# Kernel optimization log

Measured on AMD Instinct MI355X. Metric: run time of the kernel, lower is better.

Reference implementation:

```python
import jax, jax.numpy as jnp
import numpy as np

N_NODES = 20000
N_EDGES = 320000
F_IN = 512
HID = 64
N_GRAPHS = 64
N_CLASSES = 5
SLOPE = 0.2      # PyG GATConv default negative_slope
EPS_BN = 1e-5


def setup_inputs() -> dict:
    key = jax.random.key(0)
    k = jax.random.split(key, 16)
    s = 0.05
    rn = lambda kk, sh: jax.random.normal(kk, sh, jnp.float32) * s
    return {
        "x": jax.random.normal(k[0], (N_NODES, F_IN), jnp.float32),
        "edge_index": jax.random.randint(k[1], (2, N_EDGES), 0, N_NODES, jnp.int32),
        "batch": jnp.sort(jax.random.randint(k[2], (N_NODES,), 0, N_GRAPHS, jnp.int32)),
        "W1": rn(k[3], (F_IN, 4 * HID)),
        "a1_src": rn(k[4], (4, HID)), "a1_dst": rn(k[5], (4, HID)),
        "b1": jnp.zeros((4 * HID,), jnp.float32),
        "bn1_gamma": jnp.ones((4 * HID,), jnp.float32), "bn1_beta": jnp.zeros((4 * HID,), jnp.float32),
        "bn1_mean": jnp.zeros((4 * HID,), jnp.float32), "bn1_var": jnp.ones((4 * HID,), jnp.float32),
        "W2": rn(k[6], (4 * HID, 4 * HID)),
        "a2_src": rn(k[7], (4, HID)), "a2_dst": rn(k[8], (4, HID)),
        "b2": jnp.zeros((4 * HID,), jnp.float32),
        "bn2_gamma": jnp.ones((4 * HID,), jnp.float32), "bn2_beta": jnp.zeros((4 * HID,), jnp.float32),
        "bn2_mean": jnp.zeros((4 * HID,), jnp.float32), "bn2_var": jnp.ones((4 * HID,), jnp.float32),
        "W3": rn(k[9], (4 * HID, HID)),
        "a3_src": rn(k[10], (1, HID)), "a3_dst": rn(k[11], (1, HID)),
        "b3": jnp.zeros((HID,), jnp.float32),
        "lin1_w": rn(k[12], (HID, HID // 2)), "lin1_b": jnp.zeros((HID // 2,), jnp.float32),
        "lin2_w": rn(k[13], (HID // 2, N_CLASSES)), "lin2_b": jnp.zeros((N_CLASSES,), jnp.float32),
    }


def _gat(x, src, dst, W, a_s, a_d, b, heads, concat):
    """PyG-style GATConv (eval mode, self-loops already in src/dst)."""
    n = x.shape[0]
    h = (x @ W).reshape(n, heads, -1)                         # [N,H,C]
    al_s = (h * a_s).sum(-1)                                  # [N,H]
    al_d = (h * a_d).sum(-1)                                  # [N,H]
    e = jax.nn.leaky_relu(al_s[src] + al_d[dst], SLOPE)       # [E,H]
    m = jax.lax.stop_gradient(jax.ops.segment_max(e, dst, num_segments=n))
    ee = jnp.exp(e - m[dst])
    denom = jax.ops.segment_sum(ee, dst, num_segments=n)      # [N,H]
    alpha = ee / (denom[dst] + 1e-16)                         # segment softmax over dst
    out = jax.ops.segment_sum(h[src] * alpha[:, :, None], dst, num_segments=n)  # [N,H,C]
    out = out.reshape(n, -1) if concat else out.mean(axis=1)
    return out + b


def _bn(x, g, b, m, v):  # BatchNorm1d, eval mode
    return (x - m) * jax.lax.rsqrt(v + EPS_BN) * g + b


def reference(x, edge_index, batch, W1, a1_src, a1_dst, b1, bn1_gamma, bn1_beta, bn1_mean, bn1_var, W2, a2_src, a2_dst, b2, bn2_gamma, bn2_beta, bn2_mean, bn2_var, W3, a3_src, a3_dst, b3, lin1_w, lin1_b, lin2_w, lin2_b):
    n = x.shape[0]
    loops = jnp.arange(n, dtype=edge_index.dtype)             # GATConv add_self_loops=True
    src = jnp.concatenate([edge_index[0], loops])
    dst = jnp.concatenate([edge_index[1], loops])
    h = _gat(x, src, dst, W1, a1_src, a1_dst, b1, 4, True)
    h = jax.nn.relu(_bn(h, bn1_gamma, bn1_beta, bn1_mean, bn1_var))
    h = _gat(h, src, dst, W2, a2_src, a2_dst, b2, 4, True)
    h = jax.nn.relu(_bn(h, bn2_gamma, bn2_beta, bn2_mean, bn2_var))
    h = jax.nn.relu(_gat(h, src, dst, W3, a3_src, a3_dst, b3, 1, False))
    sums = jax.ops.segment_sum(h, batch, num_segments=N_GRAPHS)
    cnt = jax.ops.segment_sum(jnp.ones((n, 1), h.dtype), batch, num_segments=N_GRAPHS)
    g = sums / jnp.maximum(cnt, 1.0)                          # global_mean_pool
    g = jax.nn.relu(g @ lin1_w + lin1_b)
    return g @ lin2_w + lin2_b
```

## Files before the change

### kernel.cpp

```cpp
#include <hip/hip_runtime.h>

#define N_NODES 20000
#define N_EDGES 320000
#define E_TOT   340000
#define N_GRAPHS 64
#define N_CLASSES 5
#define SLOPE 0.2f
#define EPS_BN 1e-5f

#define CB 96
#define NCH 209

typedef _Float16 v8h __attribute__((ext_vector_type(8)));
typedef float v4f __attribute__((ext_vector_type(4)));
typedef _Float16 v4h __attribute__((ext_vector_type(4)));

#define SPQ (N_NODES * 512 / 4)
#define W1E (512 * 256)
#define W2E (256 * 256)
#define W3E (256 * 64)
#define ALZ (80000 * 4 + 20000 * 2)
#define PREP_IDS (SPQ + W1E + W2E + W3E + N_NODES + N_NODES + N_GRAPHS * 64 + ALZ)

#define RELBASE 384
#define CTRL_INTS (RELBASE + 3 * 256)

__global__ __launch_bounds__(256) void k_prep(const float* __restrict__ x,
                                              _Float16* __restrict__ xh,
                                              const float* __restrict__ W1, _Float16* __restrict__ bt1,
                                              const float* __restrict__ W2, _Float16* __restrict__ bt2,
                                              const float* __restrict__ W3, _Float16* __restrict__ bt3,
                                              const int* __restrict__ batch, int* __restrict__ gstart,
                                              int* __restrict__ cnt, float* __restrict__ sums,
                                              float* __restrict__ albase) {
    int id = blockIdx.x * 256 + threadIdx.x;
    if (id < SPQ) {
        const float4 v = *(const float4*)(x + (size_t)id * 4);
        v4h h;
        h.x = (_Float16)v.x; h.y = (_Float16)v.y; h.z = (_Float16)v.z; h.w = (_Float16)v.w;
        *(v4h*)(xh + (size_t)id * 4) = h;
        return;
    }
    id -= SPQ;
    if (id < W1E) {
        const int K = 512, N = 256;
        int n = id / K, k = id - n * K;
        bt1[id] = (_Float16)W1[(size_t)k * N + n];
        return;
    }
    id -= W1E;
    if (id < W2E) {
        const int K = 256, N = 256;
        int n = id / K, k = id - n * K;
        bt2[id] = (_Float16)W2[(size_t)k * N + n];
        return;
    }
    id -= W2E;
    if (id < W3E) {
        const int K = 256, N = 64;
        int n = id / K, k = id - n * K;
        bt3[id] = (_Float16)W3[(size_t)k * N + n];
        return;
    }
    id -= W3E;
    if (id < N_NODES) {
        int i = id;
        int b = batch[i];
        if (i == 0) {
            for (int g = 0; g <= b; ++g) gstart[g] = 0;
        } else {
            int p = batch[i - 1];
            for (int g = p + 1; g <= b; ++g) gstart[g] = i;
        }
        if (i == N_NODES - 1) {
            for (int g = b + 1; g <= N_GRAPHS; ++g) gstart[g] = N_NODES;
        }
        return;
    }
    id -= N_NODES;
    if (id < N_NODES) { cnt[id] = 0; return; }
    id -= N_NODES;
    if (id < N_GRAPHS * 64) { sums[id] = 0.f; return; }
    id -= N_GRAPHS * 64;
    if (id < ALZ) albase[id] = 0.f;
}

__device__ __forceinline__ void gsync96(int* ctrl, int k, int bid) {
    int* arr = ctrl + k * CB;
    int* rel = ctrl + RELBASE + k * 256;
    __syncthreads();
    if (threadIdx.x == 0) {
        __builtin_amdgcn_fence(__ATOMIC_RELEASE, "agent");
        __hip_atomic_store(&arr[bid], 1, __ATOMIC_RELAXED, __HIP_MEMORY_SCOPE_AGENT);
    }
    if (bid == 0) {
        if ((int)threadIdx.x < CB) {
            while (__hip_atomic_load(&arr[threadIdx.x], __ATOMIC_RELAXED, __HIP_MEMORY_SCOPE_AGENT) == 0)
                __builtin_amdgcn_s_sleep(8);
        }
        __syncthreads();
        if (threadIdx.x < 8) {
            __hip_atomic_store(&rel[threadIdx.x * 32], 1, __ATOMIC_RELAXED, __HIP_MEMORY_SCOPE_AGENT);
        }
        if (threadIdx.x == 0)
            __builtin_amdgcn_fence(__ATOMIC_ACQUIRE, "agent");
    } else if (threadIdx.x == 0) {
        int* myrel = &rel[(bid & 7) * 32];
        while (__hip_atomic_load(myrel, __ATOMIC_RELAXED, __HIP_MEMORY_SCOPE_AGENT) == 0)
            __builtin_amdgcn_s_sleep(8);
        __builtin_amdgcn_fence(__ATOMIC_ACQUIRE, "agent");
    }
    __syncthreads();
}

__device__ void csr_build(const int* __restrict__ ei, int* __restrict__ cnt,
                          int* __restrict__ wptr, int* __restrict__ indptr,
                          int* __restrict__ esrc, int* __restrict__ blocksum,
                          int* __restrict__ ctrl, int bid, int tid, int* ssc) {
    for (int e = bid * 256 + tid; e < E_TOT; e += CB * 256) {
        int d = (e < N_EDGES) ? ei[N_EDGES + e] : (e - N_EDGES);
        atomicAdd(&cnt[d], 1);
    }
    gsync96(ctrl, 0, bid);
    const int i = bid * NCH + tid;
    const int active = (tid < NCH && i < N_NODES);
    int ls = active ? cnt[i] : 0;
    ssc[tid] = ls;
    __syncthreads();
    for (int off = 1; off < 256; off <<= 1) {
        int v = (tid >= off) ? ssc[tid - off] : 0;
        __syncthreads();
        ssc[tid] += v;
        __syncthreads();
    }
    const int epre = ssc[tid] - ls;
    if (tid == 255) blocksum[bid] = ssc[255];
    gsync96(ctrl, 1, bid);
    int boff = 0;
    for (int j = 0; j < bid; ++j) boff += blocksum[j];
    if (active) {
        const int run = boff + epre;
        indptr[i] = run;
        wptr[i] = run;
    }
    if (bid == 0 && tid == 0) indptr[N_NODES] = E_TOT;
    gsync96(ctrl, 2, bid);
    for (int e = bid * 256 + tid; e < E_TOT; e += CB * 256) {
        int s, d;
        if (e < N_EDGES) { s = ei[e]; d = ei[N_EDGES + e]; }
        else             { s = d = e - N_EDGES; }
        int pos = atomicAdd(&wptr[d], 1);
        esrc[pos] = s;
    }
}

template <int TN, int KK>
__device__ void gemm_tile(const _Float16* __restrict__ A,
                          const _Float16* __restrict__ Bt,
                          _Float16* __restrict__ H,
                          const float* __restrict__ aw_s,
                          const float* __restrict__ aw_d,
                          float* __restrict__ als,
                          float* __restrict__ ald,
                          int HS, int N, int bx, int by, _Float16* lbh) {
    constexpr int NTB = 2 * TN;
    constexpr int NFRAG = 2 * NTB * 64;
    constexpr int NITER = NFRAG / 256;
    const int tid = threadIdx.x;
    const int wave = tid >> 6, lane = tid & 63;
    const int wr = wave >> 1, wc = wave & 1;
    const int q = lane >> 4, r = lane & 15;
    const int m0 = bx * 64 + wr * 32;
    const int n0 = by * (NTB * 16);
    size_t abase[2];
#pragma unroll
    for (int mi = 0; mi < 2; ++mi) {
        int ar = m0 + mi * 16 + r;
        if (ar >= N_NODES) ar = N_NODES - 1;
        abase[mi] = (size_t)ar * KK + q * 8;
    }
    size_t gaddr[NITER];
    int loff[NITER];
#pragma unroll
    for (int j = 0; j < NITER; ++j) {
        const int f = tid + j * 256;
        const int qq = f & 3;
        const int ss = (f >> 2) & 1;
        const int rr = (f >> 3) & 15;
        const int tt = f >> 7;
        gaddr[j] = (size_t)(n0 + tt * 16 + rr) * KK + ss * 32 + qq * 8;
        const int fi = (ss * NTB + tt) * 64 + qq * 16 + rr;
        loff[j] = fi * 8 + (fi >> 4) * 8;
    }
    v4f acc[2][TN];
#pragma unroll
    for (int mi = 0; mi < 2; ++mi)
#pragma unroll
        for (int t = 0; t < TN; ++t) acc[mi][t] = (v4f){0.f, 0.f, 0.f, 0.f};

    v8h ch[NITER];
#pragma unroll
    for (int j = 0; j < NITER; ++j) ch[j] = *(const v8h*)(Bt + gaddr[j]);

#pragma unroll
    for (int kc = 0; kc < KK; kc += 64) {
        __syncthreads();
#pragma unroll
        for (int j = 0; j < NITER; ++j) *(v8h*)&lbh[loff[j]] = ch[j];
        __syncthreads();
        if (kc + 64 < KK) {
#pragma unroll
            for (int j = 0; j < NITER; ++j) ch[j] = *(const v8h*)(Bt + gaddr[j] + kc + 64);
        }
#pragma unroll
        for (int ss = 0; ss < 2; ++ss) {
            v8h ah[2];
#pragma unroll
            for (int mi = 0; mi < 2; ++mi)
                ah[mi] = *(const v8h*)(A + abase[mi] + kc + ss * 32);
#pragma unroll
            for (int t = 0; t < TN; ++t) {
                const int fib = (ss * NTB + wc * TN + t) * 4 + q;
                const int off = (fib * 16 + r) * 8 + fib * 8;
                const v8h bh = *(const v8h*)&lbh[off];
#pragma unroll
                for (int mi = 0; mi < 2; ++mi)
                    acc[mi][t] = __builtin_amdgcn_mfma_f32_16x16x32_f16(ah[mi], bh, acc[mi][t], 0, 0, 0);
            }
        }
    }
#pragma unroll
    for (int mi = 0; mi < 2; ++mi)
#pragma unroll
        for (int t = 0; t < TN; ++t)
#pragma unroll
            for (int i = 0; i < 4; ++i) {
                const int row = m0 + mi * 16 + q * 4 + i;
                if (row < N_NODES) H[(size_t)row * N + n0 + (wc * TN + t) * 16 + r] = (_Float16)acc[mi][t][i];
            }
    const int colbase = n0 + wc * TN * 16;
    const int hd = colbase >> 6;
#pragma unroll
    for (int mi = 0; mi < 2; ++mi)
#pragma unroll
        for (int i = 0; i < 4; ++i) {
            float sp = 0.f, dp = 0.f;
#pragma unroll
            for (int t = 0; t < TN; ++t) {
                const int col = colbase + t * 16 + r;
                sp += acc[mi][t][i] * aw_s[col];
                dp += acc[mi][t][i] * aw_d[col];
            }
#pragma unroll
            for (int m = 1; m < 16; m <<= 1) {
                sp += __shfl_xor(sp, m, 64);
                dp += __shfl_xor(dp, m, 64);
            }
            const int row = m0 + mi * 16 + q * 4 + i;
            if (r == 0 && row < N_NODES) {
                atomicAdd(&als[row * HS + hd], sp);
                atomicAdd(&ald[row * HS + hd], dp);
            }
        }
}

__global__ __launch_bounds__(256) void k_p1(const int* __restrict__ ei,
                                            int* __restrict__ cnt, int* __restrict__ wptr,
                                            int* __restrict__ indptr, int* __restrict__ esrc,
                                            int* __restrict__ blocksum, int* __restrict__ ctrl,
                                            const _Float16* __restrict__ xh,
                                            const _Float16* __restrict__ bt1,
                                            _Float16* __restrict__ bufH,
                                            const float* __restrict__ a1s,
                                            const float* __restrict__ a1d,
                                            float* __restrict__ als1, float* __restrict__ ald1) {
    __shared__ __align__(16) char smraw[17472];
    const int bid = blockIdx.x;
    const int tid = threadIdx.x;
    if (bid < CB) {
        csr_build(ei, cnt, wptr, indptr, esrc, blocksum, ctrl, bid, tid, (int*)smraw);
    } else {
        const int t = bid - CB;
        if (t < 626) gemm_tile<4, 512>(xh, bt1, bufH, a1s, a1d, als1, ald1, 4, 256,
                                       t >> 1, t & 1, (_Float16*)smraw);
    }
}

template <int TN, int KK>
__global__ __launch_bounds__(256) void k_gemm(const _Float16* __restrict__ A,
                                              const _Float16* __restrict__ Bt,
                                              _Float16* __restrict__ H,
                                              const float* __restrict__ aw_s,
                                              const float* __restrict__ aw_d,
                                              float* __restrict__ als,
                                              float* __restrict__ ald,
                                              int HS, int N) {
    __shared__ __align__(16) char smraw[17472];
    gemm_tile<TN, KK>(A, Bt, H, aw_s, aw_d, als, ald, HS, N,
                      blockIdx.x, blockIdx.y, (_Float16*)smraw);
}

__global__ __launch_bounds__(256) void k_agg4(const _Float16* __restrict__ hin,
                                              const float* __restrict__ als,
                                              const float* __restrict__ ald,
                                              const int* __restrict__ indptr,
                                              const int* __restrict__ esrc,
                                              const float* __restrict__ bias,
                                              const float* __restrict__ gamma,
                                              const float* __restrict__ beta,
                                              const float* __restrict__ mean,
                                              const float* __restrict__ var,
                                              _Float16* __restrict__ pho) {
    __shared__ float lacc[2][64][4];
    __shared__ float lsm[2][64];
    const int pair = threadIdx.x >> 7;
    const int wv   = (threadIdx.x >> 6) & 1;
    const int lane = threadIdx.x & 63;
    const int n = blockIdx.x * 2 + pair;
    const int beg = indptr[n], end = indptr[n + 1];
    const int mid = beg + ((end - beg + 1) >> 1);
    const int e0 = wv ? mid : beg;
    const int e1 = wv ? end : mid;
    const int head = lane >> 4;
    const float aldn = ald[n * 4 + head];
    float4 acc = {0.f, 0.f, 0.f, 0.f};
    float sm = 0.f;
    const int c = lane * 4;
    int e = e0;
    for (; e + 3 < e1; e += 4) {
        const int s0 = esrc[e], s1 = esrc[e + 1], s2 = esrc[e + 2], s3 = esrc[e + 3];
        float v0 = als[s0 * 4 + head] + aldn;
        float v1 = als[s1 * 4 + head] + aldn;
        float v2 = als[s2 * 4 + head] + aldn;
        float v3 = als[s3 * 4 + head] + aldn;
        const v4h h0 = *(const v4h*)(hin + (size_t)s0 * 256 + c);
        const v4h h1 = *(const v4h*)(hin + (size_t)s1 * 256 + c);
        const v4h h2 = *(const v4h*)(hin + (size_t)s2 * 256 + c);
        const v4h h3 = *(const v4h*)(hin + (size_t)s3 * 256 + c);
        v0 = (v0 > 0.f) ? v0 : SLOPE * v0;
        v1 = (v1 > 0.f) ? v1 : SLOPE * v1;
        v2 = (v2 > 0.f) ? v2 : SLOPE * v2;
        v3 = (v3 > 0.f) ? v3 : SLOPE * v3;
        const float a0 = __expf(v0), a1 = __expf(v1), a2 = __expf(v2), a3 = __expf(v3);
        sm += (a0 + a1) + (a2 + a3);
        acc.x += a0 * (float)h0.x + a1 * (float)h1.x + a2 * (float)h2.x + a3 * (float)h3.x;
        acc.y += a0 * (float)h0.y + a1 * (float)h1.y + a2 * (float)h2.y + a3 * (float)h3.y;
        acc.z += a0 * (float)h0.z + a1 * (float)h1.z + a2 * (float)h2.z + a3 * (float)h3.z;
        acc.w += a0 * (float)h0.w + a1 * (float)h1.w + a2 * (float)h2.w + a3 * (float)h3.w;
    }
    for (; e < e1; ++e) {
        const int s0 = esrc[e];
        float v0 = als[s0 * 4 + head] + aldn;
        const v4h h0 = *(const v4h*)(hin + (size_t)s0 * 256 + c);
        v0 = (v0 > 0.f) ? v0 : SLOPE * v0;
        const float a0 = __expf(v0);
        sm += a0;
        acc.x += a0 * (float)h0.x; acc.y += a0 * (float)h0.y;
        acc.z += a0 * (float)h0.z; acc.w += a0 * (float)h0.w;
    }
    if (wv == 1) {
        lacc[pair][lane][0] = acc.x; lacc[pair][lane][1] = acc.y;
        lacc[pair][lane][2] = acc.z; lacc[pair][lane][3] = acc.w;
        lsm[pair][lane] = sm;
    }
    __syncthreads();
    if (wv == 0) {
        acc.x += lacc[pair][lane][0]; acc.y += lacc[pair][lane][1];
        acc.z += lacc[pair][lane][2]; acc.w += lacc[pair][lane][3];
        sm += lsm[pair][lane];
        const float invd = 1.f / (sm + 1e-16f);
        float y[4] = {acc.x * invd, acc.y * invd, acc.z * invd, acc.w * invd};
        v4h oh;
#pragma unroll
        for (int i = 0; i < 4; ++i) {
            float t = y[i] + bias[c + i];
            t = (t - mean[c + i]) * rsqrtf(var[c + i] + EPS_BN) * gamma[c + i] + beta[c + i];
            t = fmaxf(t, 0.f);
            oh[i] = (_Float16)t;
        }
        *(v4h*)(pho + (size_t)n * 256 + c) = oh;
    }
}

__global__ __launch_bounds__(256) void k_agg1(const _Float16* __restrict__ hin,
                                              const float* __restrict__ als,
                                              const float* __restrict__ ald,
                                              const int* __restrict__ indptr,
                                              const int* __restrict__ esrc,
                                              const float* __restrict__ bias,
                                              const int* __restrict__ batch,
                                              float* __restrict__ sums) {
    const int n = blockIdx.x * 4 + (threadIdx.x >> 6);
    const int lane = threadIdx.x & 63;
    const int beg = indptr[n], end = indptr[n + 1];
    const float aldn = ald[n];
    float acc = 0.f, sm = 0.f;
    int e = beg;
    for (; e + 3 < end; e += 4) {
        const int s0 = esrc[e], s1 = esrc[e + 1], s2 = esrc[e + 2], s3 = esrc[e + 3];
        float v0 = als[s0] + aldn;
        float v1 = als[s1] + aldn;
        float v2 = als[s2] + aldn;
        float v3 = als[s3] + aldn;
        const float h0 = (float)hin[(size_t)s0 * 64 + lane];
        const float h1 = (float)hin[(size_t)s1 * 64 + lane];
        const float h2 = (float)hin[(size_t)s2 * 64 + lane];
        const float h3 = (float)hin[(size_t)s3 * 64 + lane];
        v0 = (v0 > 0.f) ? v0 : SLOPE * v0;
        v1 = (v1 > 0.f) ? v1 : SLOPE * v1;
        v2 = (v2 > 0.f) ? v2 : SLOPE * v2;
        v3 = (v3 > 0.f) ? v3 : SLOPE * v3;
        const float a0 = __expf(v0), a1 = __expf(v1), a2 = __expf(v2), a3 = __expf(v3);
        sm += (a0 + a1) + (a2 + a3);
        acc += a0 * h0 + a1 * h1 + a2 * h2 + a3 * h3;
    }
    for (; e < end; ++e) {
        const int s0 = esrc[e];
        float v0 = als[s0] + aldn;
        const float h0 = (float)hin[(size_t)s0 * 64 + lane];
        v0 = (v0 > 0.f) ? v0 : SLOPE * v0;
        const float a0 = __expf(v0);
        sm += a0;
        acc += a0 * h0;
    }
    const float invd = 1.f / (sm + 1e-16f);
    const float val = fmaxf(acc * invd + bias[lane], 0.f);
    atomicAdd(&sums[batch[n] * 64 + lane], val);
}

__global__ void k_mlp(const float* __restrict__ sums, const int* __restrict__ gstart,
                      const float* __restrict__ w1, const float* __restrict__ b1,
                      const float* __restrict__ w2, const float* __restrict__ b2,
                      float* __restrict__ outp) {
    const int g = blockIdx.x;
    const int t = threadIdx.x;
    __shared__ float hid[32];
    const int cntn = gstart[g + 1] - gstart[g];
    const float inv = 1.f / (float)max(cntn, 1);
    float acc = b1[t];
    for (int c = 0; c < 64; ++c) acc += (sums[g * 64 + c] * inv) * w1[c * 32 + t];
    hid[t] = fmaxf(acc, 0.f);
    __syncthreads();
    if (t < N_CLASSES) {
        float o = b2[t];
        for (int k = 0; k < 32; ++k) o += hid[k] * w2[k * 5 + t];
        outp[g * 5 + t] = o;
    }
}

extern "C" void kernel_launch(void* const* d_in, const int* in_sizes, int n_in,
                              void* d_out, int out_size, void* d_ws, size_t ws_size,
                              hipStream_t stream) {
    const float* x        = (const float*)d_in[0];
    const int* edge_index = (const int*)d_in[1];
    const int* batch      = (const int*)d_in[2];
    const float* W1  = (const float*)d_in[3];
    const float* a1s = (const float*)d_in[4];
    const float* a1d = (const float*)d_in[5];
    const float* b1  = (const float*)d_in[6];
    const float* g1  = (const float*)d_in[7];
    const float* be1 = (const float*)d_in[8];
    const float* mu1 = (const float*)d_in[9];
    const float* va1 = (const float*)d_in[10];
    const float* W2  = (const float*)d_in[11];
    const float* a2s = (const float*)d_in[12];
    const float* a2d = (const float*)d_in[13];
    const float* b2  = (const float*)d_in[14];
    const float* g2  = (const float*)d_in[15];
    const float* be2 = (const float*)d_in[16];
    const float* mu2 = (const float*)d_in[17];
    const float* va2 = (const float*)d_in[18];
    const float* W3  = (const float*)d_in[19];
    const float* a3s = (const float*)d_in[20];
    const float* a3d = (const float*)d_in[21];
    const float* b3  = (const float*)d_in[22];
    const float* l1w = (const float*)d_in[23];
    const float* l1b = (const float*)d_in[24];
    const float* l2w = (const float*)d_in[25];
    const float* l2b = (const float*)d_in[26];
    float* out = (float*)d_out;

    char* w = (char*)d_ws;
    size_t off = 0;
    auto alloc = [&](size_t bytes) -> void* {
        void* p = w + off;
        off += (bytes + 255) & ~(size_t)255;
        return p;
    };
    _Float16* xh   = (_Float16*)alloc((size_t)N_NODES * 512 * 2);
    _Float16* phf  = xh;
    _Float16* bufH  = (_Float16*)alloc((size_t)N_NODES * 256 * 2);
    _Float16* bufH3 = (_Float16*)alloc((size_t)N_NODES * 64 * 2);
    _Float16* bt1 = (_Float16*)alloc((size_t)512 * 256 * 2);
    _Float16* bt2 = (_Float16*)alloc((size_t)256 * 256 * 2);
    _Float16* bt3 = (_Float16*)alloc((size_t)256 * 64 * 2);
    float* albase = (float*)alloc((size_t)ALZ * 4);
    float* als1 = albase;
    float* ald1 = albase + 80000;
    float* als2 = albase + 160000;
    float* ald2 = albase + 240000;
    float* als3 = albase + 320000;
    float* ald3 = albase + 340000;
    int* cnt      = (int*)alloc((size_t)N_NODES * 4);
    int* wptr     = (int*)alloc((size_t)N_NODES * 4);
    int* indptr   = (int*)alloc((size_t)(N_NODES + 1) * 4);
    int* esrc     = (int*)alloc((size_t)E_TOT * 4);
    int* gstart   = (int*)alloc((size_t)(N_GRAPHS + 1) * 4);
    float* sums   = (float*)alloc((size_t)N_GRAPHS * 64 * 4);
    int* blocksum = (int*)alloc((size_t)CB * 4);
    int* ctrl     = (int*)alloc((size_t)CTRL_INTS * 4);

    hipMemsetAsync(ctrl, 0, (size_t)CTRL_INTS * 4, stream);

    k_prep<<<(PREP_IDS + 255) / 256, 256, 0, stream>>>(x, xh, W1, bt1, W2, bt2, W3, bt3,
                                                       batch, gstart, cnt, sums, albase);
    k_p1<<<CB + 626, 256, 0, stream>>>(edge_index, cnt, wptr, indptr, esrc, blocksum, ctrl,
                                       xh, bt1, bufH, a1s, a1d, als1, ald1);
    k_agg4<<<N_NODES / 2, 256, 0, stream>>>(bufH, als1, ald1, indptr, esrc, b1, g1, be1, mu1, va1, phf);
    k_gemm<4, 256><<<dim3(313, 2), 256, 0, stream>>>(phf, bt2, bufH, a2s, a2d, als2, ald2, 4, 256);
    k_agg4<<<N_NODES / 2, 256, 0, stream>>>(bufH, als2, ald2, indptr, esrc, b2, g2, be2, mu2, va2, phf);
    k_gemm<2, 256><<<dim3(313, 1), 256, 0, stream>>>(phf, bt3, bufH3, a3s, a3d, als3, ald3, 1, 64);
    k_agg1<<<N_NODES / 4, 256, 0, stream>>>(bufH3, als3, ald3, indptr, esrc, b3, batch, sums);
    k_mlp<<<N_GRAPHS, 32, 0, stream>>>(sums, gstart, l1w, l1b, l2w, l2b, out);
}
```

Measured before the change: 311.3 us.

## Use one wave per node in aggregation, narrower GEMM tiles, deeper gather unroll

The 4-head aggregation kernel now gives each node a single wavefront instead of splitting its edges across two waves, which removes the LDS reduction and the block barrier. The gather loops in both aggregation kernels are unrolled to 8 edges so more independent loads are in flight per wave. The layer-1 and layer-2 GEMMs switch from TN=4 to TN=2 tiles with twice as many blocks, and their LDS arrays are sized per template, which should lower LDS use and raise occupancy. The trade-off is less parallelism per node on high-degree nodes and less operand reuse per GEMM tile.

```diff
diff --git a/kernel.cpp b/kernel.cpp
--- a/kernel.cpp
+++ b/kernel.cpp
@@ -264,6 +264,9 @@
         }
 }
 
+template <int TN>
+struct LdsSize { static constexpr int halfs = (2 * 2 * TN * 64) * 8 + ((2 * 2 * TN * 64) >> 4) * 8; };
+
 __global__ __launch_bounds__(256) void k_p1(const int* __restrict__ ei,
                                             int* __restrict__ cnt, int* __restrict__ wptr,
                                             int* __restrict__ indptr, int* __restrict__ esrc,
@@ -274,15 +277,15 @@
                                             const float* __restrict__ a1s,
                                             const float* __restrict__ a1d,
                                             float* __restrict__ als1, float* __restrict__ ald1) {
-    __shared__ __align__(16) char smraw[17472];
+    __shared__ __align__(16) _Float16 lbh[LdsSize<2>::halfs];
     const int bid = blockIdx.x;
     const int tid = threadIdx.x;
     if (bid < CB) {
-        csr_build(ei, cnt, wptr, indptr, esrc, blocksum, ctrl, bid, tid, (int*)smraw);
+        csr_build(ei, cnt, wptr, indptr, esrc, blocksum, ctrl, bid, tid, (int*)lbh);
     } else {
         const int t = bid - CB;
-        if (t < 626) gemm_tile<4, 512>(xh, bt1, bufH, a1s, a1d, als1, ald1, 4, 256,
-                                       t >> 1, t & 1, (_Float16*)smraw);
+        if (t < 1252) gemm_tile<2, 512>(xh, bt1, bufH, a1s, a1d, als1, ald1, 4, 256,
+                                        t >> 2, t & 3, lbh);
     }
 }
 
@@ -295,9 +298,9 @@
                                               float* __restrict__ als,
                                               float* __restrict__ ald,
                                               int HS, int N) {
-    __shared__ __align__(16) char smraw[17472];
+    __shared__ __align__(16) _Float16 lbh[LdsSize<TN>::halfs];
     gemm_tile<TN, KK>(A, Bt, H, aw_s, aw_d, als, ald, HS, N,
-                      blockIdx.x, blockIdx.y, (_Float16*)smraw);
+                      blockIdx.x, blockIdx.y, lbh);
 }
 
 __global__ __launch_bounds__(256) void k_agg4(const _Float16* __restrict__ hin,
@@ -311,44 +314,35 @@
                                               const float* __restrict__ mean,
                                               const float* __restrict__ var,
                                               _Float16* __restrict__ pho) {
-    __shared__ float lacc[2][64][4];
-    __shared__ float lsm[2][64];
-    const int pair = threadIdx.x >> 7;
-    const int wv   = (threadIdx.x >> 6) & 1;
+    const int n = blockIdx.x * 4 + (threadIdx.x >> 6);
     const int lane = threadIdx.x & 63;
-    const int n = blockIdx.x * 2 + pair;
+    const int head = lane >> 4;
+    const int c = lane * 4;
     const int beg = indptr[n], end = indptr[n + 1];
-    const int mid = beg + ((end - beg + 1) >> 1);
-    const int e0 = wv ? mid : beg;
-    const int e1 = wv ? end : mid;
-    const int head = lane >> 4;
     const float aldn = ald[n * 4 + head];
     float4 acc = {0.f, 0.f, 0.f, 0.f};
     float sm = 0.f;
-    const int c = lane * 4;
-    int e = e0;
-    for (; e + 3 < e1; e += 4) {
-        const int s0 = esrc[e], s1 = esrc[e + 1], s2 = esrc[e + 2], s3 = esrc[e + 3];
-        float v0 = als[s0 * 4 + head] + aldn;
-        float v1 = als[s1 * 4 + head] + aldn;
-        float v2 = als[s2 * 4 + head] + aldn;
-        float v3 = als[s3 * 4 + head] + aldn;
-        const v4h h0 = *(const v4h*)(hin + (size_t)s0 * 256 + c);
-        const v4h h1 = *(const v4h*)(hin + (size_t)s1 * 256 + c);
-        const v4h h2 = *(const v4h*)(hin + (size_t)s2 * 256 + c);
-        const v4h h3 = *(const v4h*)(hin + (size_t)s3 * 256 + c);
-        v0 = (v0 > 0.f) ? v0 : SLOPE * v0;
-        v1 = (v1 > 0.f) ? v1 : SLOPE * v1;
-        v2 = (v2 > 0.f) ? v2 : SLOPE * v2;
-        v3 = (v3 > 0.f) ? v3 : SLOPE * v3;
-        const float a0 = __expf(v0), a1 = __expf(v1), a2 = __expf(v2), a3 = __expf(v3);
-        sm += (a0 + a1) + (a2 + a3);
-        acc.x += a0 * (float)h0.x + a1 * (float)h1.x + a2 * (float)h2.x + a3 * (float)h3.x;
-        acc.y += a0 * (float)h0.y + a1 * (float)h1.y + a2 * (float)h2.y + a3 * (float)h3.y;
-        acc.z += a0 * (float)h0.z + a1 * (float)h1.z + a2 * (float)h2.z + a3 * (float)h3.z;
-        acc.w += a0 * (float)h0.w + a1 * (float)h1.w + a2 * (float)h2.w + a3 * (float)h3.w;
-    }
-    for (; e < e1; ++e) {
+    int e = beg;
+    for (; e + 7 < end; e += 8) {
+        int s[8]; float vv[8]; v4h hh[8];
+#pragma unroll
+        for (int j = 0; j < 8; ++j) s[j] = esrc[e + j];
+#pragma unroll
+        for (int j = 0; j < 8; ++j) {
+            vv[j] = als[s[j] * 4 + head] + aldn;
+            hh[j] = *(const v4h*)(hin + (size_t)s[j] * 256 + c);
+        }
+#pragma unroll
+        for (int j = 0; j < 8; ++j) {
+            float v = vv[j];
+            v = (v > 0.f) ? v : SLOPE * v;
+            const float a0 = __expf(v);
+            sm += a0;
+            acc.x += a0 * (float)hh[j].x; acc.y += a0 * (float)hh[j].y;
+            acc.z += a0 * (float)hh[j].z; acc.w += a0 * (float)hh[j].w;
+        }
+    }
+    for (; e < end; ++e) {
         const int s0 = esrc[e];
         float v0 = als[s0 * 4 + head] + aldn;
         const v4h h0 = *(const v4h*)(hin + (size_t)s0 * 256 + c);
@@ -358,28 +352,17 @@
         acc.x += a0 * (float)h0.x; acc.y += a0 * (float)h0.y;
         acc.z += a0 * (float)h0.z; acc.w += a0 * (float)h0.w;
     }
-    if (wv == 1) {
-        lacc[pair][lane][0] = acc.x; lacc[pair][lane][1] = acc.y;
-        lacc[pair][lane][2] = acc.z; lacc[pair][lane][3] = acc.w;
-        lsm[pair][lane] = sm;
-    }
-    __syncthreads();
-    if (wv == 0) {
-        acc.x += lacc[pair][lane][0]; acc.y += lacc[pair][lane][1];
-        acc.z += lacc[pair][lane][2]; acc.w += lacc[pair][lane][3];
-        sm += lsm[pair][lane];
-        const float invd = 1.f / (sm + 1e-16f);
-        float y[4] = {acc.x * invd, acc.y * invd, acc.z * invd, acc.w * invd};
-        v4h oh;
-#pragma unroll
-        for (int i = 0; i < 4; ++i) {
-            float t = y[i] + bias[c + i];
-            t = (t - mean[c + i]) * rsqrtf(var[c + i] + EPS_BN) * gamma[c + i] + beta[c + i];
-            t = fmaxf(t, 0.f);
-            oh[i] = (_Float16)t;
-        }
-        *(v4h*)(pho + (size_t)n * 256 + c) = oh;
-    }
+    const float invd = 1.f / (sm + 1e-16f);
+    float y[4] = {acc.x * invd, acc.y * invd, acc.z * invd, acc.w * invd};
+    v4h oh;
+#pragma unroll
+    for (int i = 0; i < 4; ++i) {
+        float t = y[i] + bias[c + i];
+        t = (t - mean[c + i]) * rsqrtf(var[c + i] + EPS_BN) * gamma[c + i] + beta[c + i];
+        t = fmaxf(t, 0.f);
+        oh[i] = (_Float16)t;
+    }
+    *(v4h*)(pho + (size_t)n * 256 + c) = oh;
 }
 
 __global__ __launch_bounds__(256) void k_agg1(const _Float16* __restrict__ hin,
@@ -396,23 +379,23 @@
     const float aldn = ald[n];
     float acc = 0.f, sm = 0.f;
     int e = beg;
-    for (; e + 3 < end; e += 4) {
-        const int s0 = esrc[e], s1 = esrc[e + 1], s2 = esrc[e + 2], s3 = esrc[e + 3];
-        float v0 = als[s0] + aldn;
-        float v1 = als[s1] + aldn;
-        float v2 = als[s2] + aldn;
-        float v3 = als[s3] + aldn;
-        const float h0 = (float)hin[(size_t)s0 * 64 + lane];
-        const float h1 = (float)hin[(size_t)s1 * 64 + lane];
-        const float h2 = (float)hin[(size_t)s2 * 64 + lane];
-        const float h3 = (float)hin[(size_t)s3 * 64 + lane];
-        v0 = (v0 > 0.f) ? v0 : SLOPE * v0;
-        v1 = (v1 > 0.f) ? v1 : SLOPE * v1;
-        v2 = (v2 > 0.f) ? v2 : SLOPE * v2;
-        v3 = (v3 > 0.f) ? v3 : SLOPE * v3;
-        const float a0 = __expf(v0), a1 = __expf(v1), a2 = __expf(v2), a3 = __expf(v3);
-        sm += (a0 + a1) + (a2 + a3);
-        acc += a0 * h0 + a1 * h1 + a2 * h2 + a3 * h3;
+    for (; e + 7 < end; e += 8) {
+        int s[8]; float vv[8]; float hh[8];
+#pragma unroll
+        for (int j = 0; j < 8; ++j) s[j] = esrc[e + j];
+#pragma unroll
+        for (int j = 0; j < 8; ++j) {
+            vv[j] = als[s[j]] + aldn;
+            hh[j] = (float)hin[(size_t)s[j] * 64 + lane];
+        }
+#pragma unroll
+        for (int j = 0; j < 8; ++j) {
+            float v = vv[j];
+            v = (v > 0.f) ? v : SLOPE * v;
+            const float a0 = __expf(v);
+            sm += a0;
+            acc += a0 * hh[j];
+        }
     }
     for (; e < end; ++e) {
         const int s0 = esrc[e];
@@ -514,11 +497,11 @@
 
     k_prep<<<(PREP_IDS + 255) / 256, 256, 0, stream>>>(x, xh, W1, bt1, W2, bt2, W3, bt3,
                                                        batch, gstart, cnt, sums, albase);
-    k_p1<<<CB + 626, 256, 0, stream>>>(edge_index, cnt, wptr, indptr, esrc, blocksum, ctrl,
-                                       xh, bt1, bufH, a1s, a1d, als1, ald1);
-    k_agg4<<<N_NODES / 2, 256, 0, stream>>>(bufH, als1, ald1, indptr, esrc, b1, g1, be1, mu1, va1, phf);
-    k_gemm<4, 256><<<dim3(313, 2), 256, 0, stream>>>(phf, bt2, bufH, a2s, a2d, als2, ald2, 4, 256);
-    k_agg4<<<N_NODES / 2, 256, 0, stream>>>(bufH, als2, ald2, indptr, esrc, b2, g2, be2, mu2, va2, phf);
+    k_p1<<<CB + 1252, 256, 0, stream>>>(edge_index, cnt, wptr, indptr, esrc, blocksum, ctrl,
+                                        xh, bt1, bufH, a1s, a1d, als1, ald1);
+    k_agg4<<<N_NODES / 4, 256, 0, stream>>>(bufH, als1, ald1, indptr, esrc, b1, g1, be1, mu1, va1, phf);
+    k_gemm<2, 256><<<dim3(313, 4), 256, 0, stream>>>(phf, bt2, bufH, a2s, a2d, als2, ald2, 4, 256);
+    k_agg4<<<N_NODES / 4, 256, 0, stream>>>(bufH, als2, ald2, indptr, esrc, b2, g2, be2, mu2, va2, phf);
     k_gemm<2, 256><<<dim3(313, 1), 256, 0, stream>>>(phf, bt3, bufH3, a3s, a3d, als3, ald3, 1, 64);
     k_agg1<<<N_NODES / 4, 256, 0, stream>>>(bufH3, als3, ald3, indptr, esrc, b3, batch, sums);
     k_mlp<<<N_GRAPHS, 32, 0, stream>>>(sums, gstart, l1w, l1b, l2w, l2b, out);
```

Result: slower. 332.3 us (+6.7%).
